# Performance work log

Hardware: AMD Instinct MI355X
Metric: run time of the kernel (lower is better)

The kernel has to match this reference:

```python
import jax, jax.numpy as jnp
import numpy as np

TAU = 0.02
M = 5  # len(modality_types) + 1; modality 0 == padding


def setup_inputs() -> dict:
    B, Q, S, D = 64, 32, 256, 128
    key = jax.random.key(0)
    k0, k1, k2, k3, k4 = jax.random.split(key, 5)
    q = jax.random.normal(k0, (B, Q, D), dtype=jnp.float32)
    q = q / jnp.linalg.norm(q, axis=-1, keepdims=True)
    d = jax.random.normal(k1, (B, S, D), dtype=jnp.float32)
    d = d / jnp.linalg.norm(d, axis=-1, keepdims=True)
    # guarantee every modality 0..M-1 appears in each doc (first M tokens)
    head = jnp.tile(jnp.arange(M, dtype=jnp.int32), (B, 1))
    rest = jax.random.randint(k2, (B, S - M), 0, M, dtype=jnp.int32)
    modality_ids = jnp.concatenate([head, rest], axis=1)
    query_types = jax.random.randint(k3, (B,), 1, M, dtype=jnp.int32)  # in [1, M-1]
    lengths = jax.random.randint(k4, (B,), Q // 2, Q + 1)
    query_mask = jnp.arange(Q)[None, :] < lengths[:, None]
    return {"query_emb": q, "doc_emb": d, "modality_ids": modality_ids,
            "query_types": query_types, "query_mask": query_mask}


def _loss(query_emb, doc_emb, modality_ids, query_types, query_mask):
    B = query_emb.shape[0]
    idx = jnp.arange(B)
    # token-level similarity: (B, C, Q, S)
    base = jnp.einsum('bqd,csd->bcqs', query_emb, doc_emb)
    qnorm = jnp.maximum(query_mask.sum(axis=1), 1).astype(base.dtype)  # (B,)

    # agg (ColBERT max-sim): max over non-pad doc tokens, masked query sum
    nonpad = (modality_ids != 0)[None, :, None, :]
    agg_max = jnp.where(nonpad, base, -jnp.inf).max(axis=-1)           # (B, C, Q)
    sim = (agg_max * query_mask[:, None, :].astype(base.dtype)).sum(axis=-1)
    sim = sim / qnorm[:, None]                                          # (B, C)

    # _all_modality_sims: segmented max over s per modality, then sum over q
    per_mod = []
    for m in range(M):
        mask_m = (modality_ids == m)[None, :, None, :]
        per_mod.append(jnp.where(mask_m, base, -jnp.inf).max(axis=-1).sum(axis=-1))
    sims = jnp.stack(per_mod, axis=-1)                                  # (B, C, M)
    sims = sims / qnorm[:, None, None]

    # replace diagonal with the query's own modality score
    sim_fixed = sim.at[idx, idx].set(sims[idx, idx, query_types])

    # hard negatives: all (doc, modality) pairs except pad modality and own positive
    all_modal = sims.reshape(B, B * M)
    keep_mask = jnp.ones((B, B * M), dtype=bool)
    keep_mask = keep_mask.at[:, 0::M].set(False)
    keep_mask = keep_mask.at[idx, idx * M + query_types].set(False)
    n_keep = B * M - B - 1  # exact per-row count (query_types >= 1, no overlap)
    order = jnp.argsort((~keep_mask).astype(jnp.int32), axis=1, stable=True)[:, :n_keep]
    extras = jnp.take_along_axis(all_modal, order, axis=1)              # (B, n_keep)

    logits = jnp.concatenate([sim_fixed, extras], axis=1) / TAU
    # cross entropy with labels = arange(B) (positive is column b)
    return (jax.nn.logsumexp(logits, axis=1) - logits[idx, idx]).mean()


def reference(query_emb, doc_emb, modality_ids, query_types, query_mask):
    return _loss(query_emb, doc_emb, modality_ids, query_types, query_mask)
```

## Files before the change

### kernel.cpp

```cpp
#include <hip/hip_runtime.h>
#include <math.h>

#define TAU_F 0.02f
#define NB 64
#define NQ 32
#define NS 256
#define ND 128
#define MAXT 12
#define PERMSTRIDE 384

typedef __bf16 bf16x8 __attribute__((ext_vector_type(8)));
typedef float f32x16 __attribute__((ext_vector_type(16)));

#define OFF_SIMOUT 0u
#define OFF_RED    81920u

__device__ inline bf16x8 cvt2(float4 a, float4 b) {
    bf16x8 o;
    o[0] = (__bf16)a.x; o[1] = (__bf16)a.y; o[2] = (__bf16)a.z; o[3] = (__bf16)a.w;
    o[4] = (__bf16)b.x; o[5] = (__bf16)b.y; o[6] = (__bf16)b.z; o[7] = (__bf16)b.w;
    return o;
}

__global__ __launch_bounds__(256, 2) void
main_kernel(const float* __restrict__ qemb, const float* __restrict__ demb,
            const int* __restrict__ mod, const int* __restrict__ qmask,
            float* __restrict__ simout, int* __restrict__ red) {
    int blk = blockIdx.x;
    int xcd = blk & 7;
    int idx = blk >> 3;
    int c   = xcd * 8 + (idx & 7);
    int bq  = idx >> 3;
    int tid = threadIdx.x;
    int lane = tid & 63, wv = tid >> 6;
    int li32 = lane & 31, kh = lane >> 5;
    int b0 = bq * 8 + wv * 2;

    if (blk == 0 && tid == 0) { red[0] = 0; ((float*)red)[16] = 0.f; }

    bf16x8 bfrag[2][8];
#pragma unroll
    for (int bi = 0; bi < 2; ++bi)
#pragma unroll
        for (int kc = 0; kc < 8; ++kc) {
            const float* src = qemb + ((size_t)(b0 + bi) * NQ + li32) * ND + kc * 16 + kh * 8;
            float4 a = *(const float4*)src;
            float4 b = *(const float4*)(src + 4);
            bfrag[bi][kc] = cvt2(a, b);
        }

    __shared__ int sperm[PERMSTRIDE];
    __shared__ int wcnt[4][4];
    __shared__ int counts[5], firsts[5], offs[5], padded[5];
    __shared__ int stilemod[MAXT];
    __shared__ int sT;

    int m_tok = mod[c * NS + tid];
    int rank_w = 0;
#pragma unroll
    for (int m = 1; m <= 4; ++m) {
        unsigned long long bal = __ballot(m_tok == m);
        if (lane == 0) wcnt[wv][m - 1] = __popcll(bal);
        if (m_tok == m) rank_w = __popcll(bal & ((1ull << lane) - 1ull));
    }
    __syncthreads();
    if (tid == 0) {
        int pos = 0;
        for (int m = 1; m <= 4; ++m) {
            int cnt = wcnt[0][m-1] + wcnt[1][m-1] + wcnt[2][m-1] + wcnt[3][m-1];
            counts[m] = cnt;
            offs[m] = pos;
            int p = (cnt + 31) & ~31;
            padded[m] = p;
            for (int t = pos >> 5; t < (pos + p) >> 5; ++t) stilemod[t] = m;
            pos += p;
        }
        sT = pos >> 5;
    }
    __syncthreads();
    if (m_tok) {
        int rank = rank_w;
        for (int w = 0; w < wv; ++w) rank += wcnt[w][m_tok - 1];
        sperm[offs[m_tok] + rank] = tid;
        if (rank == 0) firsts[m_tok] = tid;
    }
    __syncthreads();
    if (tid < 4) {
        int m = tid + 1;
        for (int p = counts[m]; p < padded[m]; ++p) sperm[offs[m] + p] = firsts[m];
    }
    __syncthreads();
    int T = sT;

    __shared__ __bf16 sbuf[2][8 * 64 * 8];
    int row = tid & 31, chunk = tid >> 5;
    const float* drow_base = demb + (size_t)c * NS * ND + chunk * 16;

    {
        int srow = sperm[row];
        const float4* s = (const float4*)(drow_base + (size_t)srow * ND);
        float4 a0 = s[0], a1 = s[1], a2 = s[2], a3 = s[3];
        *(bf16x8*)&sbuf[0][((chunk * 64) + row) * 8]      = cvt2(a0, a1);
        *(bf16x8*)&sbuf[0][((chunk * 64) + 32 + row) * 8] = cvt2(a2, a3);
    }
    __syncthreads();

    float vmax[2][4];
#pragma unroll
    for (int bi = 0; bi < 2; ++bi)
#pragma unroll
        for (int m = 0; m < 4; ++m) vmax[bi][m] = -1e30f;

    int cur = 0;
    for (int t = 0; t < T; ++t) {
        float4 a0, a1, a2, a3;
        bool pf = (t + 1 < T);
        if (pf) {
            int srow = sperm[(t + 1) * 32 + row];
            const float4* s = (const float4*)(drow_base + (size_t)srow * ND);
            a0 = s[0]; a1 = s[1]; a2 = s[2]; a3 = s[3];
        }

        int tm = stilemod[t];
        f32x16 acc0 = {0.f,0.f,0.f,0.f,0.f,0.f,0.f,0.f,0.f,0.f,0.f,0.f,0.f,0.f,0.f,0.f};
        f32x16 acc1 = acc0;
#pragma unroll
        for (int kc = 0; kc < 8; ++kc) {
            bf16x8 af = *(const bf16x8*)&sbuf[cur][(kc * 64 + lane) * 8];
            acc0 = __builtin_amdgcn_mfma_f32_32x32x16_bf16(af, bfrag[0][kc], acc0, 0, 0, 0);
            acc1 = __builtin_amdgcn_mfma_f32_32x32x16_bf16(af, bfrag[1][kc], acc1, 0, 0, 0);
        }
        float v0 = fmaxf(fmaxf(fmaxf(acc0[0], acc0[1]),  fmaxf(acc0[2],  acc0[3])),
                         fmaxf(fmaxf(acc0[4], acc0[5]),  fmaxf(acc0[6],  acc0[7])));
        v0 = fmaxf(v0,
             fmaxf(fmaxf(fmaxf(acc0[8], acc0[9]),  fmaxf(acc0[10], acc0[11])),
                   fmaxf(fmaxf(acc0[12], acc0[13]), fmaxf(acc0[14], acc0[15]))));
        float v1 = fmaxf(fmaxf(fmaxf(acc1[0], acc1[1]),  fmaxf(acc1[2],  acc1[3])),
                         fmaxf(fmaxf(acc1[4], acc1[5]),  fmaxf(acc1[6],  acc1[7])));
        v1 = fmaxf(v1,
             fmaxf(fmaxf(fmaxf(acc1[8], acc1[9]),  fmaxf(acc1[10], acc1[11])),
                   fmaxf(fmaxf(acc1[12], acc1[13]), fmaxf(acc1[14], acc1[15]))));
        v0 = fmaxf(v0, __shfl_xor(v0, 32, 64));
        v1 = fmaxf(v1, __shfl_xor(v1, 32, 64));
        switch (tm) {
        case 1:  vmax[0][0] = fmaxf(vmax[0][0], v0); vmax[1][0] = fmaxf(vmax[1][0], v1); break;
        case 2:  vmax[0][1] = fmaxf(vmax[0][1], v0); vmax[1][1] = fmaxf(vmax[1][1], v1); break;
        case 3:  vmax[0][2] = fmaxf(vmax[0][2], v0); vmax[1][2] = fmaxf(vmax[1][2], v1); break;
        default: vmax[0][3] = fmaxf(vmax[0][3], v0); vmax[1][3] = fmaxf(vmax[1][3], v1); break;
        }

        if (pf) {
            *(bf16x8*)&sbuf[cur ^ 1][((chunk * 64) + row) * 8]      = cvt2(a0, a1);
            *(bf16x8*)&sbuf[cur ^ 1][((chunk * 64) + 32 + row) * 8] = cvt2(a2, a3);
        }
        __syncthreads();
        cur ^= 1;
    }

    int q = lane & 31;
#pragma unroll
    for (int bi = 0; bi < 2; ++bi) {
        int b = b0 + bi;
        float m1 = vmax[bi][0], m2 = vmax[bi][1], m3 = vmax[bi][2], m4 = vmax[bi][3];
        float agg = fmaxf(fmaxf(m1, m2), fmaxf(m3, m4));
        float s0 = (qmask[b * NQ + q] != 0) ? agg : 0.f;
        float s1 = m1, s2 = m2, s3 = m3, s4 = m4;
#pragma unroll
        for (int off = 16; off >= 1; off >>= 1) {
            s0 += __shfl_xor(s0, off, 64);
            s1 += __shfl_xor(s1, off, 64);
            s2 += __shfl_xor(s2, off, 64);
            s3 += __shfl_xor(s3, off, 64);
            s4 += __shfl_xor(s4, off, 64);
        }
        if (lane == 0) {
            float* o = simout + ((size_t)b * NB + c) * 5;
            o[0] = s0; o[1] = s1; o[2] = s2; o[3] = s3; o[4] = s4;
        }
    }
}

__global__ __launch_bounds__(256) void
loss_kernel(const float* __restrict__ simout, const int* __restrict__ qtypes,
            const int* __restrict__ qmask, int* __restrict__ red,
            float* __restrict__ out) {
    int r = blockIdx.x;
    int tid = threadIdx.x;
    int lane = tid & 63, wv = tid >> 6;

    __shared__ float sv[320];
    for (int i = tid; i < 320; i += 256) sv[i] = simout[(size_t)r * 320 + i];

    __shared__ int scnt;
    if (wv == 0) {
        int on = (lane < NQ) ? (qmask[r * NQ + lane] != 0) : 0;
        unsigned long long bal = __ballot(on);
        if (lane == 0) scnt = __popcll(bal);
    }
    __syncthreads();
    int cq = scnt;
    float scale = 1.0f / (TAU_F * (float)(cq > 0 ? cq : 1));
    int skip = r * 5;

    __shared__ float wred[4];
    float mx = -1e30f;
    for (int i = tid; i < 320; i += 256)
        if (i != skip) mx = fmaxf(mx, sv[i] * scale);
#pragma unroll
    for (int off = 32; off >= 1; off >>= 1) mx = fmaxf(mx, __shfl_xor(mx, off, 64));
    if (lane == 0) wred[wv] = mx;
    __syncthreads();
    mx = fmaxf(fmaxf(wred[0], wred[1]), fmaxf(wred[2], wred[3]));

    float sum = 0.f;
    for (int i = tid; i < 320; i += 256)
        if (i != skip) sum += expf(sv[i] * scale - mx);
#pragma unroll
    for (int off = 32; off >= 1; off >>= 1) sum += __shfl_xor(sum, off, 64);
    __syncthreads();
    if (lane == 0) wred[wv] = sum;
    __syncthreads();

    if (tid == 0) {
        float tot = wred[0] + wred[1] + wred[2] + wred[3];
        float pos = sv[r * 5 + qtypes[r]] * scale;
        float lr = (logf(tot) + mx - pos) * (1.0f / NB);
        float* acc = (float*)red + 16;
        float ret = atomicAdd(acc, lr);
        int bump = 1 + (ret > 1e37f ? 1 : 0);
        int old = atomicAdd(red, bump);
        if (old == NB - 1) {
            float v = atomicAdd(acc, 0.f);
            out[0] = v;
        }
    }
}

extern "C" void kernel_launch(void* const* d_in, const int* in_sizes, int n_in,
                              void* d_out, int out_size, void* d_ws, size_t ws_size,
                              hipStream_t stream) {
    const float* qemb   = (const float*)d_in[0];
    const float* demb   = (const float*)d_in[1];
    const int*   mod    = (const int*)d_in[2];
    const int*   qtypes = (const int*)d_in[3];
    const int*   qmask  = (const int*)d_in[4];

    char* ws = (char*)d_ws;
    float* simout = (float*)(ws + OFF_SIMOUT);
    int*   red    = (int*)(ws + OFF_RED);

    main_kernel<<<512, 256, 0, stream>>>(qemb, demb, mod, qmask, simout, red);
    loss_kernel<<<NB, 256, 0, stream>>>(simout, qtypes, qmask, red, (float*)d_out);
}
```

Measured before the change: 93.07 us.

## Fuse loss reduction into main kernel via last-block-per-query-group atomic counters

Removes the separate loss kernel. Each group of 64 blocks sharing a query group bumps a counter, and the last one computes the cross-entropy for those 8 queries using acquire loads of simout. It then adds into a global accumulator, and a second counter finalizes the mean. Counters are now zeroed with a hipMemsetAsync before launch, which adds a memset operation in place of the second kernel launch. The release stores and the tail work done by the last block add some serialization.

```diff
diff --git a/kernel.cpp b/kernel.cpp
--- a/kernel.cpp
+++ b/kernel.cpp
@@ -23,9 +23,11 @@
 }
 
 __global__ __launch_bounds__(256, 2) void
-main_kernel(const float* __restrict__ qemb, const float* __restrict__ demb,
-            const int* __restrict__ mod, const int* __restrict__ qmask,
-            float* __restrict__ simout, int* __restrict__ red) {
+fused_kernel(const float* __restrict__ qemb, const float* __restrict__ demb,
+             const int* __restrict__ mod, const int* __restrict__ qtypes,
+             const int* __restrict__ qmask,
+             float* __restrict__ simout, int* __restrict__ red,
+             float* __restrict__ out) {
     int blk = blockIdx.x;
     int xcd = blk & 7;
     int idx = blk >> 3;
@@ -35,8 +37,6 @@
     int lane = tid & 63, wv = tid >> 6;
     int li32 = lane & 31, kh = lane >> 5;
     int b0 = bq * 8 + wv * 2;
-
-    if (blk == 0 && tid == 0) { red[0] = 0; ((float*)red)[16] = 0.f; }
 
     bf16x8 bfrag[2][8];
 #pragma unroll
@@ -175,61 +175,69 @@
         }
         if (lane == 0) {
             float* o = simout + ((size_t)b * NB + c) * 5;
-            o[0] = s0; o[1] = s1; o[2] = s2; o[3] = s3; o[4] = s4;
-        }
-    }
-}
-
-__global__ __launch_bounds__(256) void
-loss_kernel(const float* __restrict__ simout, const int* __restrict__ qtypes,
-            const int* __restrict__ qmask, int* __restrict__ red,
-            float* __restrict__ out) {
-    int r = blockIdx.x;
-    int tid = threadIdx.x;
-    int lane = tid & 63, wv = tid >> 6;
-
-    __shared__ float sv[320];
-    for (int i = tid; i < 320; i += 256) sv[i] = simout[(size_t)r * 320 + i];
-
-    __shared__ int scnt;
-    if (wv == 0) {
-        int on = (lane < NQ) ? (qmask[r * NQ + lane] != 0) : 0;
-        unsigned long long bal = __ballot(on);
-        if (lane == 0) scnt = __popcll(bal);
-    }
-    __syncthreads();
-    int cq = scnt;
-    float scale = 1.0f / (TAU_F * (float)(cq > 0 ? cq : 1));
-    int skip = r * 5;
-
+            __hip_atomic_store(&o[0], s0, __ATOMIC_RELEASE, __HIP_MEMORY_SCOPE_AGENT);
+            __hip_atomic_store(&o[1], s1, __ATOMIC_RELEASE, __HIP_MEMORY_SCOPE_AGENT);
+            __hip_atomic_store(&o[2], s2, __ATOMIC_RELEASE, __HIP_MEMORY_SCOPE_AGENT);
+            __hip_atomic_store(&o[3], s3, __ATOMIC_RELEASE, __HIP_MEMORY_SCOPE_AGENT);
+            __hip_atomic_store(&o[4], s4, __ATOMIC_RELEASE, __HIP_MEMORY_SCOPE_AGENT);
+        }
+    }
+
+    __shared__ int slast;
+    __syncthreads();
+    if (tid == 0) {
+        int old = atomicAdd(&red[32 + bq], 1);
+        slast = (old == NB - 1);
+    }
+    __syncthreads();
+    if (!slast) return;
+
+    float partial = 0.f;
+#pragma unroll
+    for (int h = 0; h < 2; ++h) {
+        int b = bq * 8 + wv * 2 + h;
+        int on = (lane < NQ) ? (qmask[b * NQ + lane] != 0) : 0;
+        int cq = __popcll(__ballot(on));
+        float scale = 1.0f / (TAU_F * (float)(cq > 0 ? cq : 1));
+        const float* sv = simout + (size_t)b * (NB * 5);
+        float v[5];
+#pragma unroll
+        for (int j = 0; j < 5; ++j)
+            v[j] = __hip_atomic_load(&sv[lane + j * 64], __ATOMIC_ACQUIRE, __HIP_MEMORY_SCOPE_AGENT);
+        int skip = b * 5;
+        float mx = -1e30f;
+#pragma unroll
+        for (int j = 0; j < 5; ++j) {
+            int i = lane + j * 64;
+            mx = fmaxf(mx, (i == skip) ? -1e30f : v[j] * scale);
+        }
+#pragma unroll
+        for (int off = 32; off >= 1; off >>= 1) mx = fmaxf(mx, __shfl_xor(mx, off, 64));
+        float sum = 0.f;
+#pragma unroll
+        for (int j = 0; j < 5; ++j) {
+            int i = lane + j * 64;
+            if (i != skip) sum += expf(v[j] * scale - mx);
+        }
+#pragma unroll
+        for (int off = 32; off >= 1; off >>= 1) sum += __shfl_xor(sum, off, 64);
+        int qt = qtypes[b];
+        int ii = b * 5 + qt, jj = ii >> 6, ll = ii & 63;
+        float vsel = (jj == 0) ? v[0] : (jj == 1) ? v[1] : (jj == 2) ? v[2]
+                   : (jj == 3) ? v[3] : v[4];
+        float pos = __shfl(vsel, ll, 64) * scale;
+        if (lane == 0) partial += logf(sum) + mx - pos;
+    }
     __shared__ float wred[4];
-    float mx = -1e30f;
-    for (int i = tid; i < 320; i += 256)
-        if (i != skip) mx = fmaxf(mx, sv[i] * scale);
-#pragma unroll
-    for (int off = 32; off >= 1; off >>= 1) mx = fmaxf(mx, __shfl_xor(mx, off, 64));
-    if (lane == 0) wred[wv] = mx;
-    __syncthreads();
-    mx = fmaxf(fmaxf(wred[0], wred[1]), fmaxf(wred[2], wred[3]));
-
-    float sum = 0.f;
-    for (int i = tid; i < 320; i += 256)
-        if (i != skip) sum += expf(sv[i] * scale - mx);
-#pragma unroll
-    for (int off = 32; off >= 1; off >>= 1) sum += __shfl_xor(sum, off, 64);
-    __syncthreads();
-    if (lane == 0) wred[wv] = sum;
-    __syncthreads();
-
+    if (lane == 0) wred[wv] = partial;
+    __syncthreads();
     if (tid == 0) {
-        float tot = wred[0] + wred[1] + wred[2] + wred[3];
-        float pos = sv[r * 5 + qtypes[r]] * scale;
-        float lr = (logf(tot) + mx - pos) * (1.0f / NB);
+        float lr = (wred[0] + wred[1] + wred[2] + wred[3]) * (1.0f / NB);
         float* acc = (float*)red + 16;
         float ret = atomicAdd(acc, lr);
         int bump = 1 + (ret > 1e37f ? 1 : 0);
         int old = atomicAdd(red, bump);
-        if (old == NB - 1) {
+        if (old == 7) {
             float v = atomicAdd(acc, 0.f);
             out[0] = v;
         }
@@ -249,6 +257,7 @@
     float* simout = (float*)(ws + OFF_SIMOUT);
     int*   red    = (int*)(ws + OFF_RED);
 
-    main_kernel<<<512, 256, 0, stream>>>(qemb, demb, mod, qmask, simout, red);
-    loss_kernel<<<NB, 256, 0, stream>>>(simout, qtypes, qmask, red, (float*)d_out);
+    hipMemsetAsync(red, 0, 256, stream);
+    fused_kernel<<<512, 256, 0, stream>>>(qemb, demb, mod, qtypes, qmask,
+                                          simout, red, (float*)d_out);
 }
```

After: 247.7 us. 166% more time.
